# Kernel optimization log

Measured on AMD Instinct MI355X. Metric: run time of the kernel, lower is better.

Reference implementation:

```python
import jax, jax.numpy as jnp
import numpy as np

DT = 0.03
SEQ_LEN = 30
STEER_RATE = 0.4
B = 2097152


def clip_by_tensor(t, t_min, t_max):
    # Faithful to original: (t>min)*t + (t<min)*min, then (r<=max)*r + (r>max)*max.
    # Note: when t == t_min the result is 0, matching the torch code's quirk.
    r = (t > t_min).astype(t.dtype) * t + (t < t_min).astype(t.dtype) * t_min
    r = (r <= t_max).astype(r.dtype) * r + (r > t_max).astype(r.dtype) * t_max
    return r


def setup_inputs() -> dict:
    key = jax.random.key(0)
    k1, k2 = jax.random.split(key)
    z = jax.random.normal(k1, (B, 2), dtype=jnp.float32)
    init_state = jax.random.normal(k2, (B, 6), dtype=jnp.float32)
    return {"z": z, "init_state": init_state}


def reference(z, init_state):
    last_st = init_state[:, 5]
    state0 = init_state[:, :4]  # [B,4] = x, y, psi, v

    steering = z[:, 1] * 0.5
    d_steer = STEER_RATE * DT
    steering = clip_by_tensor(steering, last_st - d_steer, last_st + d_steer)
    steering = jnp.clip(steering, -0.5, 0.5)
    pedal = z[:, 0] * 2.5

    # controls are constant across steps; clamps are idempotent
    beta = jnp.clip(steering, -0.5, 0.5)
    a_t = jnp.clip(pedal, -2.5, 2.5)
    tan_beta = jnp.tan(beta)

    def step(state, _):
        x_t, y_t, psi_t, v_t = state[:, 0], state[:, 1], state[:, 2], state[:, 3]
        v_t1 = jnp.clip(v_t + a_t * DT, 0.0, 10.0)
        psi_t1 = (v_t * tan_beta / 2.5) * DT + psi_t
        x_t1 = v_t1 * jnp.cos(psi_t1) * DT + x_t
        y_t1 = v_t1 * jnp.sin(psi_t1) * DT + y_t
        new_state = jnp.stack([x_t1, y_t1, psi_t1, v_t1], axis=1)
        return new_state, new_state

    _, traj = jax.lax.scan(step, state0, None, length=SEQ_LEN)  # [T,B,4]
    return jnp.transpose(traj, (1, 0, 2))  # [B,T,4]
```

## Files before the change

kernel.cpp:

```cpp
#include <hip/hip_runtime.h>

#define DT 0.03f
#define SEQ_LEN 30
#define D_STEER (0.4f * 0.03f)

#define BT 64
#define PAD 31

typedef float f32x2 __attribute__((ext_vector_type(2)));
typedef float f32x4 __attribute__((ext_vector_type(4)));

__global__ __launch_bounds__(64) void ccdec_kernel(
    const float* __restrict__ z,
    const float* __restrict__ init_state,
    float* __restrict__ out,
    int B)
{
    __shared__ f32x4 lds[BT * PAD];

    int tid = threadIdx.x;
    int b   = blockIdx.x * BT + tid;
    bool valid = (b < B);
    int bb = valid ? b : (B - 1);

    const f32x2* zp = reinterpret_cast<const f32x2*>(z) + (size_t)bb;
    f32x2 zv = __builtin_nontemporal_load(zp);
    const f32x2* stp = reinterpret_cast<const f32x2*>(init_state + 6ull * (size_t)bb);
    f32x2 s01 = __builtin_nontemporal_load(stp + 0);
    f32x2 s23 = __builtin_nontemporal_load(stp + 1);
    f32x2 s45 = __builtin_nontemporal_load(stp + 2);

    float x   = s01.x;
    float y   = s01.y;
    float psi = s23.x;
    float v   = s23.y;
    float last_st = s45.y;

    float steering = zv.y * 0.5f;
    float tmin = last_st - D_STEER;
    float tmax = last_st + D_STEER;
    float r = (steering > tmin) ? steering : ((steering < tmin) ? tmin : 0.0f);
    r = (r <= tmax) ? r : tmax;
    steering = fminf(fmaxf(r, -0.5f), 0.5f);

    float pedal = zv.x * 2.5f;
    float beta  = fminf(fmaxf(steering, -0.5f), 0.5f);
    float a_t   = fminf(fmaxf(pedal, -2.5f), 2.5f);
    float tan_beta = __tanf(beta);
    float dpsi_k   = tan_beta * (1.0f / 2.5f) * DT;
    float adt      = a_t * DT;

    bool full_tile = ((blockIdx.x + 1) * BT <= B);

    if (full_tile) {
        #pragma unroll
        for (int t = 0; t < SEQ_LEN; ++t) {
            float v1 = fminf(fmaxf(v + adt, 0.0f), 10.0f);
            psi = v * dpsi_k + psi;
            float s, c;
            __sincosf(psi, &s, &c);
            x = v1 * c * DT + x;
            y = v1 * s * DT + y;
            v = v1;
            f32x4 o; o.x = x; o.y = y; o.z = psi; o.w = v;
            lds[tid * PAD + t] = o;
        }
        __syncthreads();

        f32x4* outp4 = reinterpret_cast<f32x4*>(out) + (size_t)blockIdx.x * BT * SEQ_LEN;
        #pragma unroll
        for (int m = 0; m < SEQ_LEN; ++m) {
            int f  = tid + m * BT;
            int rr = f / SEQ_LEN;
            int jj = f - rr * SEQ_LEN;
            __builtin_nontemporal_store(lds[rr * PAD + jj], outp4 + f);
        }
    } else {
        if (valid) {
            f32x4* outp = reinterpret_cast<f32x4*>(out + 120ull * (size_t)b);
            #pragma unroll
            for (int t = 0; t < SEQ_LEN; ++t) {
                float v1 = fminf(fmaxf(v + adt, 0.0f), 10.0f);
                psi = v * dpsi_k + psi;
                float s, c;
                __sincosf(psi, &s, &c);
                x = v1 * c * DT + x;
                y = v1 * s * DT + y;
                v = v1;
                f32x4 o; o.x = x; o.y = y; o.z = psi; o.w = v;
                outp[t] = o;
            }
        }
    }
}

extern "C" void kernel_launch(void* const* d_in, const int* in_sizes, int n_in,
                              void* d_out, int out_size, void* d_ws, size_t ws_size,
                              hipStream_t stream)
{
    const float* z          = (const float*)d_in[0];
    const float* init_state = (const float*)d_in[1];
    float* out = (float*)d_out;

    int B = in_sizes[0] / 2;
    int blocks = (B + BT - 1) / BT;
    ccdec_kernel<<<blocks, BT, 0, stream>>>(z, init_state, out, B);
}
```

Baseline: 206.9 us.

## Switch to persistent grid looping over contiguous tile ranges, drop nontemporal hints

Launches a fixed grid of 1280 blocks instead of one block per 64-element tile. Each block walks a contiguous range of tiles, reusing its LDS staging buffer, with a barrier at the end of each iteration. Nontemporal loads and stores are replaced with plain accesses. This is meant to cut block launch and scheduling overhead, but it lowers the number of resident waves available to hide memory latency, and the loop runs serially within each block.

```diff
diff --git a/kernel.cpp b/kernel.cpp
--- a/kernel.cpp
+++ b/kernel.cpp
@@ -14,70 +14,49 @@
     const float* __restrict__ z,
     const float* __restrict__ init_state,
     float* __restrict__ out,
-    int B)
+    int B, int ntiles, int grid)
 {
     __shared__ f32x4 lds[BT * PAD];
 
-    int tid = threadIdx.x;
-    int b   = blockIdx.x * BT + tid;
-    bool valid = (b < B);
-    int bb = valid ? b : (B - 1);
+    const int tid = threadIdx.x;
 
-    const f32x2* zp = reinterpret_cast<const f32x2*>(z) + (size_t)bb;
-    f32x2 zv = __builtin_nontemporal_load(zp);
-    const f32x2* stp = reinterpret_cast<const f32x2*>(init_state + 6ull * (size_t)bb);
-    f32x2 s01 = __builtin_nontemporal_load(stp + 0);
-    f32x2 s23 = __builtin_nontemporal_load(stp + 1);
-    f32x2 s45 = __builtin_nontemporal_load(stp + 2);
+    int t0 = (int)(((long long)blockIdx.x       * ntiles) / grid);
+    int t1 = (int)(((long long)(blockIdx.x + 1) * ntiles) / grid);
 
-    float x   = s01.x;
-    float y   = s01.y;
-    float psi = s23.x;
-    float v   = s23.y;
-    float last_st = s45.y;
+    for (int tile = t0; tile < t1; ++tile) {
+        int b  = tile * BT + tid;
+        bool valid = (b < B);
+        int bb = valid ? b : (B - 1);
 
-    float steering = zv.y * 0.5f;
-    float tmin = last_st - D_STEER;
-    float tmax = last_st + D_STEER;
-    float r = (steering > tmin) ? steering : ((steering < tmin) ? tmin : 0.0f);
-    r = (r <= tmax) ? r : tmax;
-    steering = fminf(fmaxf(r, -0.5f), 0.5f);
+        f32x2 zv  = *(reinterpret_cast<const f32x2*>(z) + (size_t)bb);
+        const f32x2* stp = reinterpret_cast<const f32x2*>(init_state) + 3ull * (size_t)bb;
+        f32x2 s01 = stp[0];
+        f32x2 s23 = stp[1];
+        f32x2 s45 = stp[2];
 
-    float pedal = zv.x * 2.5f;
-    float beta  = fminf(fmaxf(steering, -0.5f), 0.5f);
-    float a_t   = fminf(fmaxf(pedal, -2.5f), 2.5f);
-    float tan_beta = __tanf(beta);
-    float dpsi_k   = tan_beta * (1.0f / 2.5f) * DT;
-    float adt      = a_t * DT;
+        float x   = s01.x;
+        float y   = s01.y;
+        float psi = s23.x;
+        float v   = s23.y;
+        float last_st = s45.y;
 
-    bool full_tile = ((blockIdx.x + 1) * BT <= B);
+        float steering = zv.y * 0.5f;
+        float tmin = last_st - D_STEER;
+        float tmax = last_st + D_STEER;
+        float r = (steering > tmin) ? steering : ((steering < tmin) ? tmin : 0.0f);
+        r = (r <= tmax) ? r : tmax;
+        steering = fminf(fmaxf(r, -0.5f), 0.5f);
 
-    if (full_tile) {
-        #pragma unroll
-        for (int t = 0; t < SEQ_LEN; ++t) {
-            float v1 = fminf(fmaxf(v + adt, 0.0f), 10.0f);
-            psi = v * dpsi_k + psi;
-            float s, c;
-            __sincosf(psi, &s, &c);
-            x = v1 * c * DT + x;
-            y = v1 * s * DT + y;
-            v = v1;
-            f32x4 o; o.x = x; o.y = y; o.z = psi; o.w = v;
-            lds[tid * PAD + t] = o;
-        }
-        __syncthreads();
+        float pedal = zv.x * 2.5f;
+        float beta  = fminf(fmaxf(steering, -0.5f), 0.5f);
+        float a_t   = fminf(fmaxf(pedal, -2.5f), 2.5f);
+        float tan_beta = __tanf(beta);
+        float dpsi_k   = tan_beta * (1.0f / 2.5f) * DT;
+        float adt      = a_t * DT;
 
-        f32x4* outp4 = reinterpret_cast<f32x4*>(out) + (size_t)blockIdx.x * BT * SEQ_LEN;
-        #pragma unroll
-        for (int m = 0; m < SEQ_LEN; ++m) {
-            int f  = tid + m * BT;
-            int rr = f / SEQ_LEN;
-            int jj = f - rr * SEQ_LEN;
-            __builtin_nontemporal_store(lds[rr * PAD + jj], outp4 + f);
-        }
-    } else {
-        if (valid) {
-            f32x4* outp = reinterpret_cast<f32x4*>(out + 120ull * (size_t)b);
+        bool full_tile = ((tile + 1) * BT <= B);
+
+        if (full_tile) {
             #pragma unroll
             for (int t = 0; t < SEQ_LEN; ++t) {
                 float v1 = fminf(fmaxf(v + adt, 0.0f), 10.0f);
@@ -88,9 +67,36 @@
                 y = v1 * s * DT + y;
                 v = v1;
                 f32x4 o; o.x = x; o.y = y; o.z = psi; o.w = v;
-                outp[t] = o;
+                lds[tid * PAD + t] = o;
+            }
+            __syncthreads();
+
+            f32x4* outp4 = reinterpret_cast<f32x4*>(out) + (size_t)tile * BT * SEQ_LEN;
+            #pragma unroll
+            for (int m = 0; m < SEQ_LEN; ++m) {
+                int f  = tid + m * BT;
+                int rr = f / SEQ_LEN;
+                int jj = f - rr * SEQ_LEN;
+                outp4[f] = lds[rr * PAD + jj];
+            }
+        } else {
+            if (valid) {
+                f32x4* outp = reinterpret_cast<f32x4*>(out) + (size_t)b * SEQ_LEN;
+                #pragma unroll
+                for (int t = 0; t < SEQ_LEN; ++t) {
+                    float v1 = fminf(fmaxf(v + adt, 0.0f), 10.0f);
+                    psi = v * dpsi_k + psi;
+                    float s, c;
+                    __sincosf(psi, &s, &c);
+                    x = v1 * c * DT + x;
+                    y = v1 * s * DT + y;
+                    v = v1;
+                    f32x4 o; o.x = x; o.y = y; o.z = psi; o.w = v;
+                    outp[t] = o;
+                }
             }
         }
+        __syncthreads();
     }
 }
 
@@ -103,6 +109,8 @@
     float* out = (float*)d_out;
 
     int B = in_sizes[0] / 2;
-    int blocks = (B + BT - 1) / BT;
-    ccdec_kernel<<<blocks, BT, 0, stream>>>(z, init_state, out, B);
+    int ntiles = (B + BT - 1) / BT;
+    int grid = 256 * 5;
+    if (grid > ntiles) grid = ntiles;
+    ccdec_kernel<<<grid, BT, 0, stream>>>(z, init_state, out, B, ntiles, grid);
 }
```

Result: slower. 223.1 us (+7.8%).
